# Kernel tuning notes

Hardware: AMD Instinct MI355X
Metric: run time of the kernel (lower is better)

Reference implementation:

```python
import jax, jax.numpy as jnp
import numpy as np

B, S, D = 4, 2048, 1024
H = 2 * D          # hidden_dim = 2*n_embd
A = H // 16        # adapt_dim = 128
E = 8              # num_experts
K = 2              # top-k within group
GS = 4             # group_size
G = E // GS        # num_groups


def _ln(x, g, b, eps=1e-5):
    m = x.mean(-1, keepdims=True)
    v = x.var(-1, keepdims=True)
    return (x - m) / jnp.sqrt(v + eps) * g + b


def setup_inputs() -> dict:
    key = jax.random.key(0)
    ks = jax.random.split(key, 12)
    s = 1.0 / np.sqrt(D)       # shared MLP init scale
    sa = s * 0.01              # adapt layers init scale
    se = 0.01 / np.sqrt(A)     # expert adapter init scale
    f32 = jnp.float32
    return {
        "x": jax.random.normal(ks[0], (B, S, D), f32),
        "W_up": jax.random.normal(ks[1], (H, D), f32) * s,
        "W_gate": jax.random.normal(ks[2], (H, D), f32) * s,
        "W_down": jax.random.normal(ks[3], (D, H), f32) * s,
        "W_pre": jax.random.normal(ks[4], (A, D), f32) * sa,
        "W_post": jax.random.normal(ks[5], (A, H), f32) * sa,
        "g_an": jnp.ones((A,), f32),
        "b_an": jnp.zeros((A,), f32),
        "W_aproj": jax.random.normal(ks[6], (H, A), f32) * sa,
        "W_eadapt": jax.random.normal(ks[7], (E, A, A), f32) * se,
        "g_e": jnp.ones((E, A), f32),
        "b_e": jnp.zeros((E, A), f32),
        "W_eproj": jax.random.normal(ks[8], (H, A), f32) * se,
        "W_oproj": jax.random.normal(ks[9], (D, H), f32) * se,
        "W_rg": jax.random.normal(ks[10], (G, D), f32) * 0.001,
        "W_re": jax.random.normal(ks[11], (GS, D), f32) * 0.001,
    }


def reference(x, W_up, W_gate, W_down, W_pre, W_post, g_an, b_an, W_aproj,
              W_eadapt, g_e, b_e, W_eproj, W_oproj, W_rg, W_re):
    Bs, Ss, Ds = x.shape
    N = Bs * Ss
    xf = x.reshape(N, Ds)

    # ---- HierarchicalRouter ----
    gl = xf @ W_rg.T                                   # [N, G]
    gp = jax.nn.softmax(gl, axis=-1)
    gw = gp.max(axis=-1)                               # top-1 group weight
    gi = gp.argmax(axis=-1)                            # top-1 group index
    ll = xf @ W_re.T                                   # [N, GS]
    lp = jax.nn.softmax(ll, axis=-1)
    lw, li = jax.lax.top_k(lp, K)                      # [N, K]
    eidx = gi[:, None] * GS + li                       # global expert ids
    lw = lw / (lw.sum(-1, keepdims=True) + 1e-7)
    fw = gw[:, None] * lw                              # final weights [N, K]
    dispatch = jnp.zeros((N, E), x.dtype).at[jnp.arange(N)[:, None], eidx].set(fw)
    load = dispatch.sum(0)
    target = load.sum() / E
    load_balance_loss = jnp.mean((load - target) ** 2)
    z_loss = jnp.mean(gl ** 2) + jnp.mean(ll ** 2)
    router_loss = 0.001 * (load_balance_loss + z_loss)

    # ---- SharedExpertMLP ----
    up = x @ W_up.T                                    # [B, S, H]
    gate = x @ W_gate.T
    hidden = jax.nn.silu(gate) * up
    pre = x @ W_pre.T                                  # [B, S, A]
    a_in = _ln(pre, g_an, b_an)
    a_out = _ln(hidden @ W_post.T, g_an, b_an)
    aw = jax.nn.silu(jnp.clip(jnp.einsum('bsa,bta->bst', a_in, a_out), -5.0, 5.0))
    adapt = jnp.einsum('bst,bta->bsa', aw, a_in) @ W_aproj.T  # [B, S, H]
    hidden = hidden + 0.1 * adapt
    shared = hidden @ W_down.T                         # [B, S, D]

    # ---- ExpertGroup (vectorized gather/MLP/scatter) ----
    # sum_i w_i * (shared + 0.1*contrib_i) = shared*sum(w) + 0.1*sum_i w_i*contrib_i
    w = dispatch.reshape(Bs, Ss, E)                    # dispatch weights
    he = jnp.einsum('bsa,eca->ebsc', pre, W_eadapt)    # [E, B, S, A]
    he = _ln(he, g_e[:, None, None, :], b_e[:, None, None, :])
    wh = jnp.einsum('ebsa,bse->bsa', he, w)            # weighted combine at adapt_dim
    contrib = (wh @ W_eproj.T) @ W_oproj.T             # [B, S, D]
    out = shared * w.sum(-1, keepdims=True) + 0.1 * contrib
    return out, router_loss
```

## Files before the change

kernel.cpp:

```cpp
#include <hip/hip_runtime.h>
#include <hip/hip_bf16.h>

typedef unsigned short u16;
typedef short bf16x8 __attribute__((ext_vector_type(8)));
typedef float f32x4 __attribute__((ext_vector_type(4)));

#define N_TOK 8192
#define DIM   1024
#define HID   2048
#define ADIM  128
#define SEQ   2048
#define LDP   2304

__device__ __forceinline__ u16 f2bf_bits(float f){
  unsigned u = __float_as_uint(f);
  unsigned r = (u + 0x7fffu + ((u >> 16) & 1u)) >> 16;
  return (u16)r;
}
__device__ __forceinline__ float bf2f(u16 v){ return __uint_as_float((unsigned)v << 16); }
__device__ __forceinline__ float siluf(float x){ return x / (1.f + __expf(-x)); }

__device__ __forceinline__ void gload16(const void* g, void* l){
  __builtin_amdgcn_global_load_lds((const __attribute__((address_space(1))) void*)g,
                                   (__attribute__((address_space(3))) void*)l, 16, 0, 0);
}


__global__ void __launch_bounds__(512, 2)
gemm_gu256(const u16* __restrict__ X, const u16* __restrict__ Wgu,
           const float* __restrict__ sumw, u16* __restrict__ hidP)
{
  extern __shared__ u16 lds[];
  const int tid = threadIdx.x, w = tid >> 6, lane = tid & 63;
  const int wm = w >> 2, wn = w & 3;
  const int swz = (blockIdx.x & 7) * 64 + (blockIdx.x >> 3);
  const int bm = swz & 31, bn = swz >> 5;
  const long brow = (long)bm * 256, bcol = (long)bn * 256;
  const int frow = lane & 15, fk = (lane >> 4) * 8;
  const int fks = fk ^ (((lane >> 1) & 3) << 3);
  const int srow = lane >> 2;
  const int sslot = (((lane & 3) ^ ((lane >> 3) & 3)) * 8);

  f32x4 acc[8][4];
  #pragma unroll
  for (int m = 0; m < 8; m++)
    #pragma unroll
    for (int n = 0; n < 4; n++)
      #pragma unroll
      for (int i = 0; i < 4; i++) acc[m][n][i] = 0.f;

  auto stage = [&](const u16* __restrict__ gbase, long row0, int kt, int kh,
                   int p, int regoff) {
    #pragma unroll
    for (int i = 0; i < 2; i++) {
      const int r = (i * 8 + w) * 16 + srow;
      const u16* g = gbase + (row0 + r) * 1024 + kt * 64 + kh * 32 + sslot;
      u16* l = &lds[p * 32768 + regoff + kh * 8192 + (i * 8 + w) * 512];
      gload16(g, l);
    }
  };

#define AFRAG(mf, kss) (*(const bf16x8*)&lds[p*32768 + (kss)*8192 + (wm*128 + (mf)*16 + frow)*32 + fks])
#define BFRAG(nf, kss) (*(const bf16x8*)&lds[p*32768 + 16384 + (kss)*8192 + (wn*64 + (nf)*16 + frow)*32 + fks])

  stage(X, brow, 0, 0, 0, 0);
  stage(Wgu, bcol, 0, 0, 0, 16384);
  stage(X, brow, 0, 1, 0, 0);
  stage(Wgu, bcol, 0, 1, 0, 16384);

  for (int kt = 0; kt < 16; ++kt) {
    const int p = kt & 1, pn = p ^ 1;
    const int ktn = (kt < 15) ? kt + 1 : 15;
    bf16x8 b0[4], b1[4], a[4];

    asm volatile("s_waitcnt vmcnt(4)" ::: "memory");
    __builtin_amdgcn_s_barrier();
    __builtin_amdgcn_sched_barrier(0);
    #pragma unroll
    for (int n = 0; n < 4; n++) b0[n] = BFRAG(n, 0);
    #pragma unroll
    for (int m = 0; m < 4; m++) a[m] = AFRAG(m, 0);
    stage(X, brow, ktn, 0, pn, 0);
    __builtin_amdgcn_s_setprio(1);
    #pragma unroll
    for (int m = 0; m < 4; m++)
      #pragma unroll
      for (int n = 0; n < 4; n++)
        acc[m][n] = __builtin_amdgcn_mfma_f32_16x16x32_bf16(a[m], b0[n], acc[m][n], 0, 0, 0);
    __builtin_amdgcn_s_setprio(0);

    __builtin_amdgcn_s_barrier();
    __builtin_amdgcn_sched_barrier(0);
    #pragma unroll
    for (int m = 0; m < 4; m++) a[m] = AFRAG(m + 4, 0);
    stage(Wgu, bcol, ktn, 0, pn, 16384);
    __builtin_amdgcn_s_setprio(1);
    #pragma unroll
    for (int m = 0; m < 4; m++)
      #pragma unroll
      for (int n = 0; n < 4; n++)
        acc[m + 4][n] = __builtin_amdgcn_mfma_f32_16x16x32_bf16(a[m], b0[n], acc[m + 4][n], 0, 0, 0);
    __builtin_amdgcn_s_setprio(0);

    asm volatile("s_waitcnt vmcnt(4)" ::: "memory");
    __builtin_amdgcn_s_barrier();
    __builtin_amdgcn_sched_barrier(0);
    #pragma unroll
    for (int n = 0; n < 4; n++) b1[n] = BFRAG(n, 1);
    #pragma unroll
    for (int m = 0; m < 4; m++) a[m] = AFRAG(m, 1);
    stage(X, brow, ktn, 1, pn, 0);
    __builtin_amdgcn_s_setprio(1);
    #pragma unroll
    for (int m = 0; m < 4; m++)
      #pragma unroll
      for (int n = 0; n < 4; n++)
        acc[m][n] = __builtin_amdgcn_mfma_f32_16x16x32_bf16(a[m], b1[n], acc[m][n], 0, 0, 0);
    __builtin_amdgcn_s_setprio(0);

    __builtin_amdgcn_s_barrier();
    __builtin_amdgcn_sched_barrier(0);
    #pragma unroll
    for (int m = 0; m < 4; m++) a[m] = AFRAG(m + 4, 1);
    stage(Wgu, bcol, ktn, 1, pn, 16384);
    __builtin_amdgcn_s_setprio(1);
    #pragma unroll
    for (int m = 0; m < 4; m++)
      #pragma unroll
      for (int n = 0; n < 4; n++)
        acc[m + 4][n] = __builtin_amdgcn_mfma_f32_16x16x32_bf16(a[m], b1[n], acc[m + 4][n], 0, 0, 0);
    __builtin_amdgcn_s_setprio(0);
  }
#undef AFRAG
#undef BFRAG

  #pragma unroll
  for (int mf = 0; mf < 8; mf++)
    #pragma unroll
    for (int i = 0; i < 4; i++) {
      const long r = brow + wm * 128 + mf * 16 + (lane >> 4) * 4 + i;
      const float sw = sumw[r];
      #pragma unroll
      for (int q = 0; q < 2; q++) {
        const float g = acc[mf][2 * q][i], u = acc[mf][2 * q + 1][i];
        const int hcol = (bn * 8 + wn * 2 + q) * 16 + (lane & 15);
        hidP[r * LDP + hcol] = f2bf_bits(sw * (siluf(g) * u));
      }
    }
}

enum { EPI_BF16 = 0, EPI_SILU = 2 };

template<int EPI>
__global__ void __launch_bounds__(256, 2)
gemm_bt(const u16* __restrict__ Ag, const u16* __restrict__ Bg, int K, int lda, int ldb,
        long sAz, long sBz, long sOz, u16* __restrict__ bout, int ldo, int col0)
{
  __shared__ u16 lA[128 * 32];
  __shared__ u16 lB[128 * 32];
  const int tid = threadIdx.x, wave = tid >> 6, lane = tid & 63;
  const long brow = (long)blockIdx.y * 128, bcol = (long)blockIdx.x * 128;
  const u16* A = Ag + (long)blockIdx.z * sAz + brow * lda;
  const u16* B = Bg + (long)blockIdx.z * sBz + bcol * ldb;
  const int wr = (wave >> 1) * 64, wc = (wave & 1) * 64;

  f32x4 acc[4][4];
  #pragma unroll
  for (int m = 0; m < 4; m++)
    #pragma unroll
    for (int n = 0; n < 4; n++)
      #pragma unroll
      for (int i = 0; i < 4; i++) acc[m][n][i] = 0.f;

  const int sr = tid >> 2, sks = ((tid & 3) ^ ((tid >> 3) & 3)) * 8;
  const u16* gA = A + (long)sr * lda + sks;
  const u16* gB = B + (long)sr * ldb + sks;
  const long rA = (long)64 * lda, rB = (long)64 * ldb;
  u16* lA0 = &lA[wave * 512]; u16* lA1 = &lA[2048 + wave * 512];
  u16* lB0 = &lB[wave * 512]; u16* lB1 = &lB[2048 + wave * 512];
  const int frow = lane & 15;
  const int fks = ((lane >> 4) * 8) ^ (((lane >> 1) & 3) << 3);

  for (int kt = 0; kt < K; kt += 32) {
    gload16(gA, lA0); gload16(gA + rA, lA1);
    gload16(gB, lB0); gload16(gB + rB, lB1);
    gA += 32; gB += 32;
    asm volatile("s_waitcnt vmcnt(0)" ::: "memory");
    __syncthreads();
    bf16x8 af[4], bfv[4];
    #pragma unroll
    for (int m = 0; m < 4; m++) af[m] = *(const bf16x8*)&lA[(wr + m * 16 + frow) * 32 + fks];
    #pragma unroll
    for (int n = 0; n < 4; n++) bfv[n] = *(const bf16x8*)&lB[(wc + n * 16 + frow) * 32 + fks];
    #pragma unroll
    for (int m = 0; m < 4; m++)
      #pragma unroll
      for (int n = 0; n < 4; n++)
        acc[m][n] = __builtin_amdgcn_mfma_f32_16x16x32_bf16(af[m], bfv[n], acc[m][n], 0, 0, 0);
    __syncthreads();
  }

  const long r0 = brow + wr + ((lane >> 4) << 2);
  const long c0 = bcol + wc + (lane & 15);
  u16* O = bout + (long)blockIdx.z * sOz;
  #pragma unroll
  for (int m = 0; m < 4; m++) {
    #pragma unroll
    for (int i = 0; i < 4; i++) {
      long r = r0 + m * 16 + i;
      #pragma unroll
      for (int n = 0; n < 4; n++) {
        long c = c0 + n * 16;
        float v = acc[m][n][i];
        if constexpr (EPI == EPI_BF16) {
          O[r * ldo + col0 + c] = f2bf_bits(v);
        } else {
          v = fminf(5.f, fmaxf(-5.f, v));
          O[r * ldo + c] = f2bf_bits(siluf(v));
        }
      }
    }
  }
}

__global__ void __launch_bounds__(256, 2)
gemm_f32(const u16* __restrict__ Ag, const u16* __restrict__ Bg,
         float* __restrict__ out)
{
  __shared__ u16 lA[128 * 32];
  __shared__ u16 lB[128 * 32];
  const int tid = threadIdx.x, wave = tid >> 6, lane = tid & 63;
  const long brow = (long)blockIdx.y * 128, bcol = (long)blockIdx.x * 128;
  const int wr = (wave >> 1) * 64, wc = (wave & 1) * 64;

  f32x4 acc[4][4];
  #pragma unroll
  for (int m = 0; m < 4; m++)
    #pragma unroll
    for (int n = 0; n < 4; n++)
      #pragma unroll
      for (int i = 0; i < 4; i++) acc[m][n][i] = 0.f;

  const int sr = tid >> 2, sks = ((tid & 3) ^ ((tid >> 3) & 3)) * 8;
  const u16* gA = Ag + brow * LDP + (long)sr * LDP + sks;
  const u16* gB = Bg + bcol * LDP + (long)sr * LDP + sks;
  const long rA = (long)64 * LDP, rB = (long)64 * LDP;
  u16* lA0 = &lA[wave * 512]; u16* lA1 = &lA[2048 + wave * 512];
  u16* lB0 = &lB[wave * 512]; u16* lB1 = &lB[2048 + wave * 512];
  const int frow = lane & 15;
  const int fks = ((lane >> 4) * 8) ^ (((lane >> 1) & 3) << 3);

  for (int kt = 0; kt < LDP; kt += 32) {
    gload16(gA, lA0); gload16(gA + rA, lA1);
    gload16(gB, lB0); gload16(gB + rB, lB1);
    gA += 32; gB += 32;
    asm volatile("s_waitcnt vmcnt(0)" ::: "memory");
    __syncthreads();
    bf16x8 af[4], bfv[4];
    #pragma unroll
    for (int m = 0; m < 4; m++) af[m] = *(const bf16x8*)&lA[(wr + m * 16 + frow) * 32 + fks];
    #pragma unroll
    for (int n = 0; n < 4; n++) bfv[n] = *(const bf16x8*)&lB[(wc + n * 16 + frow) * 32 + fks];
    #pragma unroll
    for (int m = 0; m < 4; m++)
      #pragma unroll
      for (int n = 0; n < 4; n++)
        acc[m][n] = __builtin_amdgcn_mfma_f32_16x16x32_bf16(af[m], bfv[n], acc[m][n], 0, 0, 0);
    __syncthreads();
  }

  const long r0 = brow + wr + ((lane >> 4) << 2);
  const long c0 = bcol + wc + (lane & 15);
  #pragma unroll
  for (int m = 0; m < 4; m++)
    #pragma unroll
    for (int i = 0; i < 4; i++) {
      long r = r0 + m * 16 + i;
      #pragma unroll
      for (int n = 0; n < 4; n++)
        out[r * DIM + c0 + n * 16] = acc[m][n][i];
    }
}

__global__ void __launch_bounds__(256, 2)
gemm_split(const u16* __restrict__ Ag, const u16* __restrict__ Bg, int Ksub, int nsplit,
           int lda, int ldb, long sAz, long sBz, float* __restrict__ part)
{
  __shared__ u16 lA[128 * 32];
  __shared__ u16 lB[128 * 32];
  const int tid = threadIdx.x, wave = tid >> 6, lane = tid & 63;
  const int z = blockIdx.z, batch = z / nsplit, split = z % nsplit;
  const long brow = (long)blockIdx.y * 128;
  const int Mrows = gridDim.y * 128;
  const u16* A = Ag + (long)batch * sAz + brow * lda + (long)split * Ksub;
  const u16* B = Bg + (long)batch * sBz + (long)split * Ksub;
  const int wr = (wave >> 1) * 64, wc = (wave & 1) * 64;

  f32x4 acc[4][4];
  #pragma unroll
  for (int m = 0; m < 4; m++)
    #pragma unroll
    for (int n = 0; n < 4; n++)
      #pragma unroll
      for (int i = 0; i < 4; i++) acc[m][n][i] = 0.f;

  const int sr = tid >> 2, sks = ((tid & 3) ^ ((tid >> 3) & 3)) * 8;
  const u16* gA = A + (long)sr * lda + sks;
  const u16* gB = B + (long)sr * ldb + sks;
  const long rA = (long)64 * lda, rB = (long)64 * ldb;
  u16* lA0 = &lA[wave * 512]; u16* lA1 = &lA[2048 + wave * 512];
  u16* lB0 = &lB[wave * 512]; u16* lB1 = &lB[2048 + wave * 512];
  const int frow = lane & 15;
  const int fks = ((lane >> 4) * 8) ^ (((lane >> 1) & 3) << 3);

  for (int kt = 0; kt < Ksub; kt += 32) {
    gload16(gA, lA0); gload16(gA + rA, lA1);
    gload16(gB, lB0); gload16(gB + rB, lB1);
    gA += 32; gB += 32;
    asm volatile("s_waitcnt vmcnt(0)" ::: "memory");
    __syncthreads();
    bf16x8 af[4], bfv[4];
    #pragma unroll
    for (int m = 0; m < 4; m++) af[m] = *(const bf16x8*)&lA[(wr + m * 16 + frow) * 32 + fks];
    #pragma unroll
    for (int n = 0; n < 4; n++) bfv[n] = *(const bf16x8*)&lB[(wc + n * 16 + frow) * 32 + fks];
    #pragma unroll
    for (int m = 0; m < 4; m++)
      #pragma unroll
      for (int n = 0; n < 4; n++)
        acc[m][n] = __builtin_amdgcn_mfma_f32_16x16x32_bf16(af[m], bfv[n], acc[m][n], 0, 0, 0);
    __syncthreads();
  }

  float* po = part + (long)z * Mrows * 128;
  const long rr = brow + wr + ((lane >> 4) << 2);
  const int cc = wc + (lane & 15);
  #pragma unroll
  for (int m = 0; m < 4; m++)
    #pragma unroll
    for (int i = 0; i < 4; i++) {
      long r = rr + m * 16 + i;
      #pragma unroll
      for (int n = 0; n < 4; n++)
        po[r * 128 + cc + n * 16] = acc[m][n][i];
    }
}

__global__ void wprep(const float* __restrict__ Wg, const float* __restrict__ Wu,
                      const float* __restrict__ Wd, const float* __restrict__ Wo,
                      const float* __restrict__ Wpost, const float* __restrict__ Wpre,
                      const float* __restrict__ Wead,
                      u16* __restrict__ Wgu, u16* __restrict__ WdQ,
                      u16* __restrict__ Wob, u16* __restrict__ Wpostb,
                      u16* __restrict__ Wpreb, u16* __restrict__ Weadb)
{
  long i = ((long)blockIdx.x * 256 + threadIdx.x) * 8;
  const float* s; u16* d; long so, doff;
  if (i < 4194304) {
    long j = i;
    long rp = j >> 10, c = j & 1023;
    long i32 = rp >> 5, wi = rp & 31;
    s = (wi < 16) ? Wg : Wu;
    so = (i32 * 16 + (wi & 15)) * 1024 + c;
    d = Wgu; doff = j;
  } else if (i < 6291456) {
    long j = i - 4194304;
    long r = j >> 11, c = j & 2047;
    s = Wd; so = j;
    d = WdQ; doff = r * LDP + c;
  } else if (i < 8388608) { s = Wo;    so = i - 6291456; d = Wob;    doff = so; }
  else if (i < 8650752)   { s = Wpost; so = i - 8388608; d = Wpostb; doff = so; }
  else if (i < 8781824)   { s = Wpre;  so = i - 8650752; d = Wpreb;  doff = so; }
  else                    { s = Wead;  so = i - 8781824; d = Weadb;  doff = so; }
  float4 v0 = *(const float4*)(s + so), v1 = *(const float4*)(s + so + 4);
  ushort4 p, q;
  p.x = f2bf_bits(v0.x); p.y = f2bf_bits(v0.y); p.z = f2bf_bits(v0.z); p.w = f2bf_bits(v0.w);
  q.x = f2bf_bits(v1.x); q.y = f2bf_bits(v1.y); q.z = f2bf_bits(v1.z); q.w = f2bf_bits(v1.w);
  *(ushort4*)(d + doff) = p;
  *(ushort4*)(d + doff + 4) = q;
}

__global__ void cvt_t2(const float* __restrict__ Wa, const float* __restrict__ We,
                       u16* __restrict__ Ta, u16* __restrict__ Te)
{
  int bid = blockIdx.x;
  const float* src = (bid < 1024) ? Wa : We;
  u16* dst = (bid < 1024) ? Ta : Te;
  int idx = (bid & 1023) * 256 + threadIdx.x;
  int c = idx >> 11, r = idx & 2047;
  dst[idx] = f2bf_bits(src[(long)r * 128 + c]);
}

__global__ void reduce_q(const float* __restrict__ part, u16* __restrict__ WdQ)
{
  int idx = blockIdx.x * 256 + threadIdx.x;
  int r = idx >> 8, c = idx & 255;
  const float* p = part + ((c < 128) ? 0 : 524288) + (long)r * 128 + (c & 127);
  float a = p[0] + p[131072] + p[262144] + p[393216];
  WdQ[(long)r * LDP + 2048 + c] = f2bf_bits(a);
}

__global__ void __launch_bounds__(256)
ln_rows_part(const float* __restrict__ part, int nsplit,
             const float* __restrict__ g, const float* __restrict__ b,
             const float* __restrict__ sumw,
             u16* __restrict__ out, u16* __restrict__ outT, u16* __restrict__ rawout)
{
  int wave = threadIdx.x >> 6, lane = threadIdx.x & 63;
  long n = (long)blockIdx.x * 4 + wave;
  long base = n * 128;
  float x0 = 0.f, x1 = 0.f;
  for (int s = 0; s < nsplit; s++) {
    x0 += part[(long)s * (N_TOK * ADIM) + base + lane];
    x1 += part[(long)s * (N_TOK * ADIM) + base + 64 + lane];
  }
  if (sumw) { float inv = 1.f / sumw[n]; x0 *= inv; x1 *= inv; }
  float s2 = x0 + x1, q = x0 * x0 + x1 * x1;
  #pragma unroll
  for (int o = 32; o; o >>= 1) { s2 += __shfl_xor(s2, o); q += __shfl_xor(q, o); }
  float m = s2 * (1.f / 128.f);
  float var = q * (1.f / 128.f) - m * m;
  float inv = rsqrtf(var + 1e-5f);
  float y0 = (x0 - m) * inv * g[lane] + b[lane];
  float y1 = (x1 - m) * inv * g[lane + 64] + b[lane + 64];
  out[base + lane] = f2bf_bits(y0);
  out[base + 64 + lane] = f2bf_bits(y1);
  if (outT) {
    long bb = n >> 11, ss = n & 2047;
    outT[(bb * 128 + lane) * 2048 + ss] = f2bf_bits(y0);
    outT[(bb * 128 + lane + 64) * 2048 + ss] = f2bf_bits(y1);
  }
  if (rawout) {
    rawout[base + lane] = f2bf_bits(x0);
    rawout[base + 64 + lane] = f2bf_bits(x1);
  }
}

__global__ void reduce_part_p1(const float* __restrict__ part,
                               const float* __restrict__ sumw, u16* __restrict__ hidP)
{
  int idx = blockIdx.x * 256 + threadIdx.x;
  int n = idx >> 5, c4 = (idx & 31) * 4;
  int batch = n >> 11, r = n & 2047;
  float4 a = {0.f, 0.f, 0.f, 0.f};
  #pragma unroll
  for (int s = 0; s < 4; s++) {
    float4 v = *(const float4*)(part + (((long)(batch * 4 + s) * 2048 + r) << 7) + c4);
    a.x += v.x; a.y += v.y; a.z += v.z; a.w += v.w;
  }
  float rs = 0.1f * sumw[n];
  ushort4 o;
  o.x = f2bf_bits(rs * a.x); o.y = f2bf_bits(rs * a.y);
  o.z = f2bf_bits(rs * a.z); o.w = f2bf_bits(rs * a.w);
  *(ushort4*)(hidP + (long)n * LDP + 2048 + c4) = o;
}

__global__ void __launch_bounds__(256)
router_kernel(const float* __restrict__ x, const float* __restrict__ Wrg,
              const float* __restrict__ Wre, float* __restrict__ sumw,
              float* __restrict__ fwv, int* __restrict__ eidxv,
              float* __restrict__ stats, u16* __restrict__ xb)
{
  __shared__ float lst[10];
  if (threadIdx.x < 10) lst[threadIdx.x] = 0.f;
  __syncthreads();
  const int wave = threadIdx.x >> 6, lane = threadIdx.x & 63;
  const float4* wg0 = (const float4*)Wrg;
  const float4* wg1 = (const float4*)(Wrg + 1024);
  const float4* we0 = (const float4*)Wre;
  const float4* we1 = (const float4*)(Wre + 1024);
  const float4* we2 = (const float4*)(Wre + 2048);
  const float4* we3 = (const float4*)(Wre + 3072);

  for (int t = 0; t < 4; t++) {
    const long n = (long)blockIdx.x * 16 + wave * 4 + t;
    const float4* xr = (const float4*)(x + n * 1024);
    float d0 = 0, d1 = 0, t0 = 0, t1 = 0, t2 = 0, t3 = 0;
    #pragma unroll
    for (int j = 0; j < 4; j++) {
      int id = j * 64 + lane;
      float4 xv = xr[id];
      ushort4 xc;
      xc.x = f2bf_bits(xv.x); xc.y = f2bf_bits(xv.y);
      xc.z = f2bf_bits(xv.z); xc.w = f2bf_bits(xv.w);
      *(ushort4*)(xb + n * 1024 + id * 4) = xc;
      float4 a;
      a = wg0[id]; d0 += xv.x * a.x + xv.y * a.y + xv.z * a.z + xv.w * a.w;
      a = wg1[id]; d1 += xv.x * a.x + xv.y * a.y + xv.z * a.z + xv.w * a.w;
      a = we0[id]; t0 += xv.x * a.x + xv.y * a.y + xv.z * a.z + xv.w * a.w;
      a = we1[id]; t1 += xv.x * a.x + xv.y * a.y + xv.z * a.z + xv.w * a.w;
      a = we2[id]; t2 += xv.x * a.x + xv.y * a.y + xv.z * a.z + xv.w * a.w;
      a = we3[id]; t3 += xv.x * a.x + xv.y * a.y + xv.z * a.z + xv.w * a.w;
    }
    #pragma unroll
    for (int o = 32; o; o >>= 1) {
      d0 += __shfl_xor(d0, o); d1 += __shfl_xor(d1, o);
      t0 += __shfl_xor(t0, o); t1 += __shfl_xor(t1, o);
      t2 += __shfl_xor(t2, o); t3 += __shfl_xor(t3, o);
    }
    if (lane == 0) {
      float mg = fmaxf(d0, d1);
      float e0 = __expf(d0 - mg), e1 = __expf(d1 - mg);
      float invg = 1.f / (e0 + e1);
      float p0 = e0 * invg, p1 = e1 * invg;
      int gi = (d1 > d0) ? 1 : 0;
      float gw = fmaxf(p0, p1);
      float l[4] = {t0, t1, t2, t3};
      float ml = fmaxf(fmaxf(l[0], l[1]), fmaxf(l[2], l[3]));
      float p[4]; float su = 0;
      #pragma unroll
      for (int i = 0; i < 4; i++) { p[i] = __expf(l[i] - ml); su += p[i]; }
      float isu = 1.f / su;
      #pragma unroll
      for (int i = 0; i < 4; i++) p[i] *= isu;
      int i1 = 0;
      #pragma unroll
      for (int i = 1; i < 4; i++) if (p[i] > p[i1]) i1 = i;
      int i2 = (i1 == 0) ? 1 : 0;
      #pragma unroll
      for (int i = 0; i < 4; i++) if (i != i1 && p[i] > p[i2]) i2 = i;
      float s2 = p[i1] + p[i2];
      float invs = 1.f / (s2 + 1e-7f);
      float f1 = gw * p[i1] * invs, f2 = gw * p[i2] * invs;
      int ea = gi * 4 + i1, eb = gi * 4 + i2;
      sumw[n] = f1 + f2;
      fwv[2 * n] = f1; fwv[2 * n + 1] = f2;
      eidxv[2 * n] = ea; eidxv[2 * n + 1] = eb;
      atomicAdd(&lst[ea], f1);
      atomicAdd(&lst[eb], f2);
      atomicAdd(&lst[8], d0 * d0 + d1 * d1);
      atomicAdd(&lst[9], t0 * t0 + t1 * t1 + t2 * t2 + t3 * t3);
    }
  }
  __syncthreads();
  if (threadIdx.x < 10) atomicAdd(&stats[threadIdx.x], lst[threadIdx.x]);
}

__global__ void init_stats(float* stats){ if (threadIdx.x < 16) stats[threadIdx.x] = 0.f; }

__global__ void finalize_loss(const float* __restrict__ stats, float* __restrict__ out)
{
  float tot = 0;
  #pragma unroll
  for (int e = 0; e < 8; e++) tot += stats[e];
  float target = tot * 0.125f;
  float lb = 0;
  #pragma unroll
  for (int e = 0; e < 8; e++) { float d = stats[e] - target; lb += d * d; }
  lb *= 0.125f;
  float z = stats[8] * (1.f / (8192.f * 2.f)) + stats[9] * (1.f / (8192.f * 4.f));
  out[0] = 0.001f * (lb + z);
}

__global__ void __launch_bounds__(256)
ln_combine(const u16* __restrict__ he, const int* __restrict__ eidxv,
           const float* __restrict__ fwv, const float* __restrict__ g_e,
           const float* __restrict__ b_e, u16* __restrict__ hidP)
{
  const int wave = threadIdx.x >> 6, lane = threadIdx.x & 63;
  const long n = (long)blockIdx.x * 4 + wave;
  float o0 = 0.f, o1 = 0.f;
  #pragma unroll
  for (int k = 0; k < 2; k++) {
    const int e = eidxv[2 * n + k];
    const float w = fwv[2 * n + k];
    const u16* row = he + ((long)e * N_TOK + n) * 128;
    float h0 = bf2f(row[lane]), h1 = bf2f(row[lane + 64]);
    float s = h0 + h1, q = h0 * h0 + h1 * h1;
    #pragma unroll
    for (int o = 32; o; o >>= 1) { s += __shfl_xor(s, o); q += __shfl_xor(q, o); }
    float m = s * (1.f / 128.f);
    float var = q * (1.f / 128.f) - m * m;
    float inv = rsqrtf(var + 1e-5f);
    o0 += w * ((h0 - m) * inv * g_e[e * 128 + lane] + b_e[e * 128 + lane]);
    o1 += w * ((h1 - m) * inv * g_e[e * 128 + lane + 64] + b_e[e * 128 + lane + 64]);
  }
  hidP[n * LDP + 2176 + lane] = f2bf_bits(0.1f * o0);
  hidP[n * LDP + 2176 + 64 + lane] = f2bf_bits(0.1f * o1);
}

extern "C" void kernel_launch(void* const* d_in, const int* in_sizes, int n_in,
                              void* d_out, int out_size, void* d_ws, size_t ws_size,
                              hipStream_t stream)
{
  (void)in_sizes; (void)n_in; (void)out_size; (void)ws_size;
  const float* x       = (const float*)d_in[0];
  const float* W_up    = (const float*)d_in[1];
  const float* W_gate  = (const float*)d_in[2];
  const float* W_down  = (const float*)d_in[3];
  const float* W_pre   = (const float*)d_in[4];
  const float* W_post  = (const float*)d_in[5];
  const float* g_an    = (const float*)d_in[6];
  const float* b_an    = (const float*)d_in[7];
  const float* W_aproj = (const float*)d_in[8];
  const float* W_ead   = (const float*)d_in[9];
  const float* g_e     = (const float*)d_in[10];
  const float* b_e     = (const float*)d_in[11];
  const float* W_eproj = (const float*)d_in[12];
  const float* W_oproj = (const float*)d_in[13];
  const float* W_rg    = (const float*)d_in[14];
  const float* W_re    = (const float*)d_in[15];
  float* out = (float*)d_out;

  char* base = (char*)d_ws; size_t off = 0;
  auto alloc = [&](size_t bytes) -> void* {
    void* p = base + off; off = (off + bytes + 255) & ~(size_t)255; return p;
  };
  u16*   xb     = (u16*)  alloc((size_t)N_TOK * DIM * 2);
  u16*   Wgu    = (u16*)  alloc((size_t)2 * HID * DIM * 2);
  u16*   WdQ    = (u16*)  alloc((size_t)DIM * LDP * 2);
  u16*   Wob    = (u16*)  alloc((size_t)DIM * HID * 2);
  u16*   Wpostb = (u16*)  alloc((size_t)ADIM * HID * 2);
  u16*   Wpreb  = (u16*)  alloc((size_t)ADIM * DIM * 2);
  u16*   WaTb   = (u16*)  alloc((size_t)ADIM * HID * 2);
  u16*   WeTb   = (u16*)  alloc((size_t)ADIM * HID * 2);
  u16*   Weadb  = (u16*)  alloc((size_t)8 * ADIM * ADIM * 2);
  u16*   hidP   = (u16*)  alloc((size_t)N_TOK * LDP * 2);
  u16*   heb    = (u16*)  alloc((size_t)8 * N_TOK * ADIM * 2);
  float* part   = (float*)heb;
  u16*   preb   = (u16*)  alloc((size_t)N_TOK * ADIM * 2);
  u16*   a_in   = (u16*)  alloc((size_t)N_TOK * ADIM * 2);
  u16*   a_inT  = (u16*)  alloc((size_t)N_TOK * ADIM * 2);
  u16*   a_out  = (u16*)  alloc((size_t)N_TOK * ADIM * 2);
  float* sumw   = (float*)alloc((size_t)N_TOK * 4);
  float* fwv    = (float*)alloc((size_t)N_TOK * 2 * 4);
  int*   eidxv  = (int*)  alloc((size_t)N_TOK * 2 * 4);
  float* stats  = (float*)alloc(64);
  u16* aw = (u16*)d_out;

  hipFuncSetAttribute((const void*)gemm_gu256,
                      hipFuncAttributeMaxDynamicSharedMemorySize, 131072);

  init_stats<<<1, 64, 0, stream>>>(stats);
  router_kernel<<<512, 256, 0, stream>>>(x, W_rg, W_re, sumw, fwv, eidxv, stats, xb);

  wprep<<<4352, 256, 0, stream>>>(W_gate, W_up, W_down, W_oproj, W_post, W_pre, W_ead,
                                  Wgu, WdQ, Wob, Wpostb, Wpreb, Weadb);
  cvt_t2<<<2048, 256, 0, stream>>>(W_aproj, W_eproj, WaTb, WeTb);

  gemm_split<<<dim3(1, 8, 4), 256, 0, stream>>>(WdQ, WaTb, 512, 4, LDP, HID, 0, 0, part);
  gemm_split<<<dim3(1, 8, 4), 256, 0, stream>>>(Wob, WeTb, 512, 4, HID, HID, 0, 0,
      part + 524288);
  reduce_q<<<1024, 256, 0, stream>>>(part, WdQ);

  gemm_gu256<<<512, 512, 131072, stream>>>(xb, Wgu, sumw, hidP);

  gemm_split<<<dim3(1, 64, 4), 256, 0, stream>>>(xb, Wpreb, 256, 4, DIM, DIM, 0, 0, part);
  ln_rows_part<<<2048, 256, 0, stream>>>(part, 4, g_an, b_an, nullptr, a_in, a_inT, preb);

  gemm_bt<EPI_BF16><<<dim3(1, 64, 8), 256, 0, stream>>>(preb, Weadb, ADIM, ADIM, ADIM,
      0, (long)ADIM * ADIM, (long)N_TOK * ADIM, heb, ADIM, 0);
  ln_combine<<<2048, 256, 0, stream>>>(heb, eidxv, fwv, g_e, b_e, hidP);

  gemm_split<<<dim3(1, 64, 4), 256, 0, stream>>>(hidP, Wpostb, 512, 4, LDP, HID, 0, 0, part);
  ln_rows_part<<<2048, 256, 0, stream>>>(part, 4, g_an, b_an, sumw, a_out, nullptr, nullptr);

  gemm_bt<EPI_SILU><<<dim3(16, 16, 4), 256, 0, stream>>>(a_in, a_out, ADIM, ADIM, ADIM,
      (long)SEQ * ADIM, (long)SEQ * ADIM, (long)SEQ * SEQ, aw, SEQ, 0);

  gemm_split<<<dim3(1, 16, 16), 256, 0, stream>>>(aw, a_inT, 512, 4, SEQ, SEQ,
      (long)SEQ * SEQ, (long)ADIM * SEQ, part);
  reduce_part_p1<<<1024, 256, 0, stream>>>(part, sumw, hidP);

  gemm_f32<<<dim3(8, 64, 1), 256, 0, stream>>>(hidP, WdQ, out);

  finalize_loss<<<1, 1, 0, stream>>>(stats, out + (size_t)N_TOK * DIM);
}
```

Baseline: 289.2 us.

## Restructure gate-up GEMM barriers into ping-pong schedule and remap block tiles per XCD

The gate/up GEMM main loop now issues LDS fragment reads and the next global-to-LDS stage before a barrier, then waits on lgkmcnt and runs the MFMA block. This moves the synchronization points so that waves staggered across the barrier can alternate memory and matrix phases. Block-to-tile mapping also changes so each XCD gets a compact 8x8 grid of tiles (a 4x2 split of the output), aiming for better L2 reuse of X and weight rows. The extra barriers per k-step add synchronization cost and could serialize waves if the staggering does not occur.

```diff
diff --git a/kernel.cpp b/kernel.cpp
--- a/kernel.cpp
+++ b/kernel.cpp
@@ -33,11 +33,12 @@
   extern __shared__ u16 lds[];
   const int tid = threadIdx.x, w = tid >> 6, lane = tid & 63;
   const int wm = w >> 2, wn = w & 3;
-  const int swz = (blockIdx.x & 7) * 64 + (blockIdx.x >> 3);
-  const int bm = swz & 31, bn = swz >> 5;
+  const int xcd = blockIdx.x & 7, lloc = blockIdx.x >> 3;
+  const int bm = (xcd >> 1) * 8 + (lloc & 7);
+  const int bn = (xcd & 1) * 8 + (lloc >> 3);
   const long brow = (long)bm * 256, bcol = (long)bn * 256;
-  const int frow = lane & 15, fk = (lane >> 4) * 8;
-  const int fks = fk ^ (((lane >> 1) & 3) << 3);
+  const int frow = lane & 15;
+  const int fks = ((lane >> 4) * 8) ^ (((lane >> 1) & 3) << 3);
   const int srow = lane >> 2;
   const int sslot = (((lane & 3) ^ ((lane >> 3) & 3)) * 8);
 
@@ -67,69 +68,79 @@
   stage(Wgu, bcol, 0, 0, 0, 16384);
   stage(X, brow, 0, 1, 0, 0);
   stage(Wgu, bcol, 0, 1, 0, 16384);
+  asm volatile("s_waitcnt vmcnt(4)" ::: "memory");
+  __builtin_amdgcn_s_barrier();
 
   for (int kt = 0; kt < 16; ++kt) {
     const int p = kt & 1, pn = p ^ 1;
     const int ktn = (kt < 15) ? kt + 1 : 15;
-    bf16x8 b0[4], b1[4], a[4];
-
-    asm volatile("s_waitcnt vmcnt(4)" ::: "memory");
-    __builtin_amdgcn_s_barrier();
-    __builtin_amdgcn_sched_barrier(0);
-    #pragma unroll
-    for (int n = 0; n < 4; n++) b0[n] = BFRAG(n, 0);
+    bf16x8 b[4], a[4];
+
+    #pragma unroll
+    for (int n = 0; n < 4; n++) b[n] = BFRAG(n, 0);
     #pragma unroll
     for (int m = 0; m < 4; m++) a[m] = AFRAG(m, 0);
     stage(X, brow, ktn, 0, pn, 0);
+    __builtin_amdgcn_s_barrier();
+    asm volatile("s_waitcnt lgkmcnt(0)" ::: "memory");
+    __builtin_amdgcn_sched_barrier(0);
     __builtin_amdgcn_s_setprio(1);
     #pragma unroll
     for (int m = 0; m < 4; m++)
       #pragma unroll
       for (int n = 0; n < 4; n++)
-        acc[m][n] = __builtin_amdgcn_mfma_f32_16x16x32_bf16(a[m], b0[n], acc[m][n], 0, 0, 0);
+        acc[m][n] = __builtin_amdgcn_mfma_f32_16x16x32_bf16(a[m], b[n], acc[m][n], 0, 0, 0);
     __builtin_amdgcn_s_setprio(0);
-
-    __builtin_amdgcn_s_barrier();
-    __builtin_amdgcn_sched_barrier(0);
+    __builtin_amdgcn_s_barrier();
+
     #pragma unroll
     for (int m = 0; m < 4; m++) a[m] = AFRAG(m + 4, 0);
     stage(Wgu, bcol, ktn, 0, pn, 16384);
+    __builtin_amdgcn_s_barrier();
+    asm volatile("s_waitcnt lgkmcnt(0)" ::: "memory");
+    __builtin_amdgcn_sched_barrier(0);
     __builtin_amdgcn_s_setprio(1);
     #pragma unroll
     for (int m = 0; m < 4; m++)
       #pragma unroll
       for (int n = 0; n < 4; n++)
-        acc[m + 4][n] = __builtin_amdgcn_mfma_f32_16x16x32_bf16(a[m], b0[n], acc[m + 4][n], 0, 0, 0);
+        acc[m + 4][n] = __builtin_amdgcn_mfma_f32_16x16x32_bf16(a[m], b[n], acc[m + 4][n], 0, 0, 0);
     __builtin_amdgcn_s_setprio(0);
-
     asm volatile("s_waitcnt vmcnt(4)" ::: "memory");
     __builtin_amdgcn_s_barrier();
-    __builtin_amdgcn_sched_barrier(0);
-    #pragma unroll
-    for (int n = 0; n < 4; n++) b1[n] = BFRAG(n, 1);
+
+    #pragma unroll
+    for (int n = 0; n < 4; n++) b[n] = BFRAG(n, 1);
     #pragma unroll
     for (int m = 0; m < 4; m++) a[m] = AFRAG(m, 1);
     stage(X, brow, ktn, 1, pn, 0);
+    __builtin_amdgcn_s_barrier();
+    asm volatile("s_waitcnt lgkmcnt(0)" ::: "memory");
+    __builtin_amdgcn_sched_barrier(0);
     __builtin_amdgcn_s_setprio(1);
     #pragma unroll
     for (int m = 0; m < 4; m++)
       #pragma unroll
       for (int n = 0; n < 4; n++)
-        acc[m][n] = __builtin_amdgcn_mfma_f32_16x16x32_bf16(a[m], b1[n], acc[m][n], 0, 0, 0);
+        acc[m][n] = __builtin_amdgcn_mfma_f32_16x16x32_bf16(a[m], b[n], acc[m][n], 0, 0, 0);
     __builtin_amdgcn_s_setprio(0);
-
-    __builtin_amdgcn_s_barrier();
-    __builtin_amdgcn_sched_barrier(0);
+    __builtin_amdgcn_s_barrier();
+
     #pragma unroll
     for (int m = 0; m < 4; m++) a[m] = AFRAG(m + 4, 1);
     stage(Wgu, bcol, ktn, 1, pn, 16384);
+    __builtin_amdgcn_s_barrier();
+    asm volatile("s_waitcnt lgkmcnt(0)" ::: "memory");
+    __builtin_amdgcn_sched_barrier(0);
     __builtin_amdgcn_s_setprio(1);
     #pragma unroll
     for (int m = 0; m < 4; m++)
       #pragma unroll
       for (int n = 0; n < 4; n++)
-        acc[m + 4][n] = __builtin_amdgcn_mfma_f32_16x16x32_bf16(a[m], b1[n], acc[m + 4][n], 0, 0, 0);
+        acc[m + 4][n] = __builtin_amdgcn_mfma_f32_16x16x32_bf16(a[m], b[n], acc[m + 4][n], 0, 0, 0);
     __builtin_amdgcn_s_setprio(0);
+    asm volatile("s_waitcnt vmcnt(4)" ::: "memory");
+    __builtin_amdgcn_s_barrier();
   }
 #undef AFRAG
 #undef BFRAG
```

Measured after the change: 286.9 us. Within noise of the previous version (-0.8%).
